# Kernel tuning notes

Hardware: AMD Instinct MI355X
Metric: run time of the kernel (lower is better)

Reference implementation:

```python
import jax, jax.numpy as jnp
import numpy as np

# Model dims (match init_kwargs)
B, S, D = 4, 2048, 1024          # batch, seq, d_model
H, E, DH = 8, 4, 128             # n_heads, n_experts_attn, d_head
K = 2                            # k_attn (routed, n_expert_shared_attn=0)
NEG_INF = jnp.float32(-1e30)


def setup_inputs() -> dict:
    key = jax.random.key(0)
    ks = jax.random.split(key, 9)
    s = np.float32(1.0 / np.sqrt(D))
    return {
        "q_src": jax.random.normal(ks[0], (B, S, D), jnp.float32),
        "k_src": jax.random.normal(ks[1], (B, S, D), jnp.float32),
        "v_src": jax.random.normal(ks[2], (B, S, D), jnp.float32),
        "wq": jax.random.normal(ks[3], (H * DH, D), jnp.float32) * s,
        "wk": jax.random.normal(ks[4], (H * DH, D), jnp.float32) * s,
        "sel_v_w": jax.random.normal(ks[5], (H * E, D), jnp.float32) * s,
        "sel_o_w": jax.random.normal(ks[6], (H * E, D), jnp.float32) * s,
        "v_w": jax.random.normal(ks[7], (H, E, D, DH), jnp.float32) * s,
        "o_w": jax.random.normal(ks[8], (H, E, DH, D), jnp.float32) * np.float32(1.0 / np.sqrt(H * DH)),
        "bias_v": jnp.zeros((E,), jnp.float32),   # load-balancing bias buffer (zeros at init)
        "bias_o": jnp.zeros((E,), jnp.float32),
        # causal boolean mask, True = attend (skip_mask all True -> trimming is identity)
        "attn_mask": jnp.broadcast_to(jnp.tril(jnp.ones((S, S), bool)), (B, S, S)),
        "position_ids": jnp.broadcast_to(jnp.arange(S, dtype=jnp.int32), (B, S)),
        "skip_mask": jnp.ones((B, S), bool),
    }


def _expert_gate(x, w, bias):
    """Sigmoid gating + per-head top-k routed expert selection.
    Returns dense combine weights [b,s,h,E] (sum of sel_val * one_hot) and indices [b,s,h,K]."""
    logits = (x @ w.T).reshape(*x.shape[:-1], H, E)        # [b,s,h,E]
    sel = jax.nn.sigmoid(logits)
    # bias only affects *which* experts are picked (added under no_grad in torch)
    _, idx = jax.lax.top_k(jax.lax.stop_gradient(sel) + bias, K)  # [b,s,h,K]
    sel_val = jnp.take_along_axis(sel, idx, axis=-1)        # [b,s,h,K]
    gate = jnp.sum(jax.nn.one_hot(idx, E, dtype=sel.dtype) * sel_val[..., None], axis=-2)
    return gate, idx


def reference(q_src, k_src, v_src, wq, wk, sel_v_w, sel_o_w, v_w, o_w,
              bias_v, bias_o, attn_mask, position_ids, skip_mask):
    # scale.sqrt() applied to both q and k -> full 1/sqrt(d_head) on scores
    ssq = jnp.float32((1.0 / np.sqrt(DH)) ** 0.5)
    q = ((q_src @ wq.T) * ssq).reshape(B, S, H, DH).transpose(0, 2, 1, 3)  # [b,h,s,dh]
    k = ((k_src @ wk.T) * ssq).reshape(B, S, H, DH).transpose(0, 2, 1, 3)

    v_gate, v_idx = _expert_gate(k_src, sel_v_w, bias_v)    # V experts routed on k_src
    o_gate, o_idx = _expert_gate(q_src, sel_o_w, bias_o)    # O experts routed on q_src

    # expert-mixed V projection (cvmm): all experts then dense combine
    all_v = jnp.einsum('bsm,hemd->bshed', v_src, v_w)       # [b,s,h,E,dh]
    v = jnp.einsum('bshed,bshe->bhsd', all_v, v_gate)       # [b,h,s,dh]

    scores = jnp.einsum('bhqd,bhkd->bhqk', q, k)
    scores = jnp.where(attn_mask[:, None], scores, NEG_INF)
    attn = jax.nn.softmax(scores, axis=-1)
    out = jnp.einsum('bhqk,bhkd->bqhd', attn, v)            # [b,s,h,dh]

    # expert-mixed O projection, summed over heads
    scaled = out[..., None, :] * o_gate[..., None]          # [b,s,h,E,dh]
    res = jnp.einsum('bshed,hedm->bsm', scaled, o_w)        # [b,s,d_model]
    return res, (v_idx, o_idx)
```

## Files before the change

### kernel.cpp

```cpp
#include <hip/hip_runtime.h>
#include <cstdint>
#include <cstddef>

typedef __bf16 bf16;
typedef __bf16 bf16x4 __attribute__((ext_vector_type(4)));
typedef __bf16 bf16x8 __attribute__((ext_vector_type(8)));
typedef float  fx4    __attribute__((ext_vector_type(4)));


__device__ __forceinline__ void async16(const bf16* g, bf16* l) {
  __builtin_amdgcn_global_load_lds((const __attribute__((address_space(1))) void*)g,
                                   (__attribute__((address_space(3))) void*)l, 16, 0, 0);
}

template <int CTRL>
__device__ __forceinline__ float dppf(float x) {
  return __int_as_float(__builtin_amdgcn_update_dpp(
      0, __float_as_int(x), CTRL, 0xf, 0xf, true));
}

__global__ __launch_bounds__(256) void f32_to_bf16(const float4* __restrict__ src,
                                                   bf16x4* __restrict__ dst, int n4) {
  int i = blockIdx.x * 256 + threadIdx.x;
  if (i < n4) {
    float4 v = src[i];
    bf16x4 o;
    o[0] = (bf16)v.x; o[1] = (bf16)v.y; o[2] = (bf16)v.z; o[3] = (bf16)v.w;
    dst[i] = o;
  }
}

__global__ __launch_bounds__(256) void make_wvt(const float* __restrict__ v_w,
                                                bf16* __restrict__ wvt) {
  __shared__ float tile[64][65];
  const int he = blockIdx.z, k0 = blockIdx.x * 64, dh0 = blockIdx.y * 64;
  const float* in = v_w + (size_t)he * 1024 * 128;
  #pragma unroll
  for (int j = 0; j < 16; j++) {
    int idx = threadIdx.x + j * 256;
    int r = idx >> 6, c = idx & 63;
    tile[r][c] = in[(size_t)(k0 + r) * 128 + dh0 + c];
  }
  __syncthreads();
  const int h = he >> 2, e = he & 3;
  bf16* outp = wvt + ((size_t)(h * 128 + dh0) * 4 + e) * 1024 + k0;
  #pragma unroll
  for (int j = 0; j < 16; j++) {
    int idx = threadIdx.x + j * 256;
    int r = idx >> 6, c = idx & 63;
    outp[(size_t)r * 4096 + c] = (bf16)tile[c][r];
  }
}

__global__ __launch_bounds__(256) void make_wot(const float* __restrict__ o_w,
                                                bf16* __restrict__ wot) {
  __shared__ float tile[64][65];
  const int he = blockIdx.z, d0 = blockIdx.x * 64, dh0 = blockIdx.y * 64;
  const float* in = o_w + (size_t)he * 128 * 1024;
  #pragma unroll
  for (int j = 0; j < 16; j++) {
    int idx = threadIdx.x + j * 256;
    int r = idx >> 6, c = idx & 63;
    tile[r][c] = in[(size_t)(dh0 + r) * 1024 + d0 + c];
  }
  __syncthreads();
  bf16* outp = wot + (size_t)d0 * 4096 + he * 128 + dh0;
  #pragma unroll
  for (int j = 0; j < 16; j++) {
    int idx = threadIdx.x + j * 256;
    int r = idx >> 6, c = idx & 63;
    outp[(size_t)r * 4096 + c] = (bf16)tile[c][r];
  }
}

__global__ __launch_bounds__(256) void gating(const float* __restrict__ q_src,
                                              const float* __restrict__ k_src,
                                              const float* __restrict__ sel_v_w,
                                              const float* __restrict__ sel_o_w,
                                              const float* __restrict__ bias_v,
                                              const float* __restrict__ bias_o,
                                              float* __restrict__ gate_v,
                                              float* __restrict__ gate_o,
                                              float* __restrict__ d_out) {
  int m = blockIdx.x, g = blockIdx.y;
  const float* x = g ? q_src : k_src;
  const float* w = g ? sel_o_w : sel_v_w;
  const float* bias = g ? bias_o : bias_v;
  float* gate = g ? gate_o : gate_v;
  float* idxo = d_out + 8388608 + g * 131072;

  __shared__ float xs[1024];
  __shared__ double part_s[32][8];
  __shared__ double sel_s[32];
  int t = threadIdx.x;
  #pragma unroll
  for (int p = 0; p < 4; p++) xs[t + p * 256] = x[(size_t)m * 1024 + t + p * 256];
  __syncthreads();
  int he = t >> 3, pp = t & 7;
  const float* wrow = w + he * 1024;
  double acc = 0.0;
  for (int j = 0; j < 128; j++) { int k = pp + j * 8; acc += (double)xs[k] * (double)wrow[k]; }
  part_s[he][pp] = acc;
  __syncthreads();
  if (t < 32) {
    double tot = 0.0;
    #pragma unroll
    for (int j = 0; j < 8; j++) tot += part_s[t][j];
    sel_s[t] = 1.0 / (1.0 + exp(-tot));
  }
  __syncthreads();
  if (t < 8) {
    double v[4], vbv[4];
    #pragma unroll
    for (int e = 0; e < 4; e++) { v[e] = sel_s[t * 4 + e]; vbv[e] = v[e] + (double)bias[e]; }
    int i0 = 0;
    for (int e = 1; e < 4; e++) if (vbv[e] > vbv[i0]) i0 = e;
    int i1 = -1; double best = -1e300;
    for (int e = 0; e < 4; e++) { if (e == i0) continue; if (vbv[e] > best) { best = vbv[e]; i1 = e; } }
    float* gp = gate + ((size_t)m * 8 + t) * 4;
    #pragma unroll
    for (int e = 0; e < 4; e++) {
      float gv = 0.f;
      if (e == i0) gv = (float)v[i0];
      else if (e == i1) gv = (float)v[i1];
      gp[e] = gv;
    }
    idxo[m * 16 + t * 2 + 0] = (float)i0;
    idxo[m * 16 + t * 2 + 1] = (float)i1;
  }
}

__global__ __launch_bounds__(256) void expand_o(const bf16* __restrict__ outb,
                                                const float* __restrict__ gate_o,
                                                bf16* __restrict__ Ae) {
  int idx = blockIdx.x * 256 + threadIdx.x;
  int m = idx >> 9;
  int u = idx & 511;
  int he = u >> 4;
  int hh = he >> 2, e = he & 3;
  int dh0 = (u & 15) * 8;
  float gv = gate_o[((size_t)m * 8 + hh) * 4 + e];
  bf16x8 v = *(const bf16x8*)(outb + ((size_t)m * 8 + hh) * 128 + dh0);
  #pragma unroll
  for (int j = 0; j < 8; j++) v[j] = (bf16)((float)v[j] * gv);
  *(bf16x8*)(Ae + (size_t)m * 4096 + u * 8) = v;
}

template <int MODE>
__global__ __launch_bounds__(256) void gemm_moe(const bf16* __restrict__ Abf,
                                                const bf16* __restrict__ BT,
                                                const float* __restrict__ gate,
                                                bf16* __restrict__ Cbf,
                                                float* __restrict__ Cf32,
                                                float scale) {
  constexpr int KDIM = (MODE == 0) ? 1024 : 4096;
  constexpr int ASTRIDE = (MODE == 2) ? 4096 : 1024;
  __shared__ __align__(16) bf16 smem[32768];
  const int t = threadIdx.x;
  const int wave = t >> 6, lane = t & 63;
  const int wr = wave >> 1, wc = wave & 1;
  const int quad = lane >> 4, l16 = lane & 15;
  const int m0 = blockIdx.y * 128;
  const int n0 = blockIdx.x * 128;
  const int h = (MODE == 1) ? blockIdx.z : 0;
  const bf16* BTh = (MODE == 1) ? BT + (size_t)h * 128 * 4096 : BT;

  fx4 acc[4][4] = {};
  fx4 accT[4][4] = {};

  const int drow = lane >> 3, dch = lane & 7;

  auto stage = [&](int buf, int k0) {
    bf16* As = smem + buf * 16384;
    bf16* Bs = As + 8192;
    #pragma unroll
    for (int p = 0; p < 4; p++) {
      int row = p * 32 + wave * 8 + drow;
      int sc = dch ^ (row & 7);
      async16(BTh + (size_t)(n0 + row) * KDIM + k0 + sc * 8,
              Bs + row * 64 + dch * 8);
    }
    int col = (MODE == 1) ? (k0 & 1023) : k0;
    #pragma unroll
    for (int p = 0; p < 4; p++) {
      int row = p * 32 + wave * 8 + drow;
      int sc = dch ^ (row & 7);
      async16(Abf + (size_t)(m0 + row) * ASTRIDE + col + sc * 8,
              As + row * 64 + dch * 8);
    }
  };

  stage(0, 0);
  int buf = 0;
  for (int k0 = 0; k0 < KDIM; k0 += 64) {
    if (k0 + 64 < KDIM) {
      stage(buf ^ 1, k0 + 64);
      asm volatile("s_waitcnt vmcnt(8)" ::: "memory");
    } else {
      asm volatile("s_waitcnt vmcnt(0)" ::: "memory");
    }
    __builtin_amdgcn_s_barrier();
    asm volatile("" ::: "memory");
    const bf16* As = smem + buf * 16384;
    const bf16* Bs = As + 8192;
    #pragma unroll
    for (int kk = 0; kk < 64; kk += 32) {
      bf16x8 af[4], bfr[4];
      #pragma unroll
      for (int i = 0; i < 4; i++) {
        int ar = wr * 64 + i * 16 + l16;
        af[i]  = *(const bf16x8*)(As + ar * 64 + ((((kk >> 3) + quad) ^ (ar & 7)) * 8));
      }
      #pragma unroll
      for (int i = 0; i < 4; i++) {
        int br = wc * 64 + i * 16 + l16;
        bfr[i] = *(const bf16x8*)(Bs + br * 64 + ((((kk >> 3) + quad) ^ (br & 7)) * 8));
      }
      #pragma unroll
      for (int mi = 0; mi < 4; mi++)
        #pragma unroll
        for (int ni = 0; ni < 4; ni++)
          acc[mi][ni] = __builtin_amdgcn_mfma_f32_16x16x32_bf16(af[mi], bfr[ni], acc[mi][ni], 0, 0, 0);
    }
    if constexpr (MODE == 1) {
      if (((k0 + 64) & 1023) == 0) {
        const int e = k0 >> 10;
        #pragma unroll
        for (int mi = 0; mi < 4; mi++)
          #pragma unroll
          for (int r = 0; r < 4; r++) {
            int m = m0 + wr * 64 + mi * 16 + quad * 4 + r;
            float gv = gate[((size_t)m * 8 + h) * 4 + e];
            #pragma unroll
            for (int ni = 0; ni < 4; ni++)
              accT[mi][ni][r] += gv * acc[mi][ni][r];
          }
        #pragma unroll
        for (int mi = 0; mi < 4; mi++)
          #pragma unroll
          for (int ni = 0; ni < 4; ni++)
            #pragma unroll
            for (int j = 0; j < 4; j++) acc[mi][ni][j] = 0.f;
      }
    }
    asm volatile("" ::: "memory");
    __builtin_amdgcn_s_barrier();
    buf ^= 1;
  }

  if (MODE == 1) {
    #pragma unroll
    for (int mi = 0; mi < 4; mi++)
      #pragma unroll
      for (int ni = 0; ni < 4; ni++) {
        int nl = wc * 64 + ni * 16 + l16;
        int ml = wr * 64 + mi * 16 + quad * 4;
        bf16x4 pk;
        #pragma unroll
        for (int r = 0; r < 4; r++) pk[r] = (bf16)accT[mi][ni][r];
        *(bf16x4*)(smem + nl * 136 + ml) = pk;
      }
    __syncthreads();
    int b = m0 >> 11, s0 = m0 & 2047;
    const int row = t >> 1, base = (t & 1) * 64;
    bf16* dst = Cbf + (((size_t)(b * 8 + h) * 128) + row) * 2048 + s0 + base;
    #pragma unroll
    for (int j = 0; j < 8; j++)
      *(float4*)(dst + j * 8) = *(float4*)(smem + row * 136 + base + j * 8);
    return;
  }

  #pragma unroll
  for (int mi = 0; mi < 4; mi++)
    #pragma unroll
    for (int ni = 0; ni < 4; ni++)
      #pragma unroll
      for (int r = 0; r < 4; r++) {
        int m = m0 + wr * 64 + mi * 16 + quad * 4 + r;
        int n = n0 + wc * 64 + ni * 16 + l16;
        float v = acc[mi][ni][r] * scale;
        if (MODE == 0) {
          int b = m >> 11, s = m & 2047, hh = n >> 7, dh = n & 127;
          Cbf[(((size_t)(b * 8 + hh) * 2048 + s) << 7) + dh] = (bf16)v;
        } else {
          Cf32[(size_t)m * 1024 + n] = v;
        }
      }
}

__global__ __launch_bounds__(256) void attn_kernel(const bf16* __restrict__ qb,
                                                   const bf16* __restrict__ kb,
                                                   const bf16* __restrict__ vbT,
                                                   bf16* __restrict__ outb) {
  const int bh = blockIdx.y;
  const int b = bh >> 3, h = bh & 7;
  __shared__ __align__(16) bf16 Ks[2][64 * 128];
  __shared__ __align__(16) bf16 VTs[2][128 * 64];
  __shared__ __align__(16) bf16 Ps[4][16][72];
  const int t = threadIdx.x, wave = t >> 6, lane = t & 63;
  const int quad = lane >> 4, l16 = lane & 15;
  const bf16* qbase  = qb  + (size_t)bh * 2048 * 128;
  const bf16* kbase  = kb  + (size_t)bh * 2048 * 128;
  const bf16* vtbase = vbT + (size_t)bh * 128 * 2048;

  auto stage = [&](int buf, int kt) {
    #pragma unroll
    for (int p = 0; p < 4; p++) {
      int o = p * 4096 + wave * 1024 + lane * 16;
      int kr = o >> 8, kc = o & 255;
      async16((const bf16*)((const char*)kbase + (size_t)(kt * 64 + kr) * 256 + (kc ^ ((kr & 7) << 4))),
              (bf16*)((char*)&Ks[buf][0] + o));
    }
    #pragma unroll
    for (int p = 0; p < 4; p++) {
      int o = p * 4096 + wave * 1024 + lane * 16;
      int vr = o >> 7, vc = o & 127;
      async16((const bf16*)((const char*)vtbase + (size_t)vr * 4096 + kt * 128 + (vc ^ ((vr & 7) << 4))),
              (bf16*)((char*)&VTs[buf][0] + o));
    }
  };

  #pragma unroll 1
  for (int pass = 0; pass < 2; pass++) {
    const int qt = pass ? blockIdx.x : (31 - blockIdx.x);

    bf16x8 qf[4];
    #pragma unroll
    for (int dk = 0; dk < 4; dk++)
      qf[dk] = *(const bf16x8*)(qbase + (size_t)(qt * 64 + wave * 16 + l16) * 128 + dk * 32 + quad * 8);

    float m_run[4], l_run[4];
    fx4 acc_o[8] = {};
    #pragma unroll
    for (int r = 0; r < 4; r++) { m_run[r] = -1e30f; l_run[r] = 0.f; }

    stage(0, 0);
    int cur = 0;

    for (int kt = 0; kt <= qt; kt++) {
      if (kt < qt) {
        stage(cur ^ 1, kt + 1);
        asm volatile("s_waitcnt vmcnt(8)" ::: "memory");
      } else {
        asm volatile("s_waitcnt vmcnt(0)" ::: "memory");
      }
      __builtin_amdgcn_s_barrier();
      asm volatile("" ::: "memory");

      const char* Ksb  = (const char*)&Ks[cur][0];
      const char* VTsb = (const char*)&VTs[cur][0];

      fx4 accs[4] = {};
      __builtin_amdgcn_s_setprio(1);
      #pragma unroll
      for (int ni = 0; ni < 4; ni++)
        #pragma unroll
        for (int dk = 0; dk < 4; dk++) {
          int r = ni * 16 + l16;
          bf16x8 kf = *(const bf16x8*)(Ksb + r * 256 + ((dk * 64 + quad * 16) ^ ((r & 7) << 4)));
          accs[ni] = __builtin_amdgcn_mfma_f32_16x16x32_bf16(qf[dk], kf, accs[ni], 0, 0, 0);
        }
      __builtin_amdgcn_s_setprio(0);

      if (kt == qt) {
        #pragma unroll
        for (int ni = 0; ni < 4; ni++)
          #pragma unroll
          for (int r = 0; r < 4; r++) {
            int qr = wave * 16 + quad * 4 + r;
            int kc = ni * 16 + l16;
            if (kc > qr) accs[ni][r] = -1e30f;
          }
      }

      #pragma unroll
      for (int r = 0; r < 4; r++) {
        float mx = fmaxf(fmaxf(accs[0][r], accs[1][r]), fmaxf(accs[2][r], accs[3][r]));
        mx = fmaxf(mx, dppf<0x121>(mx));
        mx = fmaxf(mx, dppf<0x122>(mx));
        mx = fmaxf(mx, dppf<0x124>(mx));
        mx = fmaxf(mx, dppf<0x128>(mx));
        float m_new = fmaxf(m_run[r], mx);
        float alpha = __builtin_amdgcn_exp2f(m_run[r] - m_new);
        float rs = 0.f;
        #pragma unroll
        for (int ni = 0; ni < 4; ni++) {
          float p = __builtin_amdgcn_exp2f(accs[ni][r] - m_new);
          accs[ni][r] = p; rs += p;
        }
        rs += dppf<0x121>(rs);
        rs += dppf<0x122>(rs);
        rs += dppf<0x124>(rs);
        rs += dppf<0x128>(rs);
        l_run[r] = l_run[r] * alpha + rs;
        m_run[r] = m_new;
        #pragma unroll
        for (int nj = 0; nj < 8; nj++) acc_o[nj][r] *= alpha;
      }

      #pragma unroll
      for (int ni = 0; ni < 4; ni++)
        #pragma unroll
        for (int r = 0; r < 4; r++)
          Ps[wave][quad * 4 + r][ni * 16 + l16] = (bf16)accs[ni][r];

      __builtin_amdgcn_s_setprio(1);
      #pragma unroll
      for (int step = 0; step < 2; step++) {
        bf16x8 pf = *(const bf16x8*)&Ps[wave][l16][step * 32 + quad * 8];
        #pragma unroll
        for (int nj = 0; nj < 8; nj++) {
          int r = nj * 16 + l16;
          bf16x8 vf = *(const bf16x8*)(VTsb + r * 128 + ((step * 64 + quad * 16) ^ ((r & 7) << 4)));
          acc_o[nj] = __builtin_amdgcn_mfma_f32_16x16x32_bf16(pf, vf, acc_o[nj], 0, 0, 0);
        }
      }
      __builtin_amdgcn_s_setprio(0);

      asm volatile("" ::: "memory");
      __builtin_amdgcn_s_barrier();
      cur ^= 1;
    }

    #pragma unroll
    for (int nj = 0; nj < 8; nj++)
      #pragma unroll
      for (int r = 0; r < 4; r++) {
        int s = qt * 64 + wave * 16 + quad * 4 + r;
        int token = b * 2048 + s;
        float o = acc_o[nj][r] / l_run[r];
        outb[((size_t)token * 8 + h) * 128 + nj * 16 + l16] = (bf16)o;
      }
  }
}

extern "C" void kernel_launch(void* const* d_in, const int* in_sizes, int n_in,
                              void* d_out, int out_size, void* d_ws, size_t ws_size,
                              hipStream_t stream) {
  const float* q_src  = (const float*)d_in[0];
  const float* k_src  = (const float*)d_in[1];
  const float* v_src  = (const float*)d_in[2];
  const float* wq     = (const float*)d_in[3];
  const float* wk     = (const float*)d_in[4];
  const float* sel_v_w = (const float*)d_in[5];
  const float* sel_o_w = (const float*)d_in[6];
  const float* v_w    = (const float*)d_in[7];
  const float* o_w    = (const float*)d_in[8];
  const float* bias_v = (const float*)d_in[9];
  const float* bias_o = (const float*)d_in[10];
  float* out = (float*)d_out;

  char* ws = (char*)d_ws;
  size_t off = 0;
  auto alloc = [&](size_t bytes) { char* p = ws + off; off += (bytes + 255) & ~(size_t)255; return p; };
  bf16* wqb   = (bf16*)alloc((size_t)1024 * 1024 * 2);
  bf16* wkb   = (bf16*)alloc((size_t)1024 * 1024 * 2);
  bf16* wvt   = (bf16*)alloc((size_t)8 * 128 * 4 * 1024 * 2);
  bf16* wot   = (bf16*)alloc((size_t)1024 * 4096 * 2);
  float* gate_v = (float*)alloc((size_t)8192 * 32 * 4);
  float* gate_o = (float*)alloc((size_t)8192 * 32 * 4);
  bf16* qsb   = (bf16*)alloc((size_t)8192 * 1024 * 2);
  bf16* ksb   = (bf16*)alloc((size_t)8192 * 1024 * 2);
  bf16* vsb   = (bf16*)alloc((size_t)8192 * 1024 * 2);
  bf16* qb    = (bf16*)alloc((size_t)8192 * 1024 * 2);
  bf16* kb    = (bf16*)alloc((size_t)8192 * 1024 * 2);
  bf16* vbT   = (bf16*)alloc((size_t)8192 * 1024 * 2);
  bf16* outb  = (bf16*)alloc((size_t)8192 * 1024 * 2);
  bf16* Ae    = qsb;

  f32_to_bf16<<<1024, 256, 0, stream>>>((const float4*)wq, (bf16x4*)wqb, 262144);
  f32_to_bf16<<<1024, 256, 0, stream>>>((const float4*)wk, (bf16x4*)wkb, 262144);
  f32_to_bf16<<<8192, 256, 0, stream>>>((const float4*)q_src, (bf16x4*)qsb, 2097152);
  f32_to_bf16<<<8192, 256, 0, stream>>>((const float4*)k_src, (bf16x4*)ksb, 2097152);
  f32_to_bf16<<<8192, 256, 0, stream>>>((const float4*)v_src, (bf16x4*)vsb, 2097152);
  make_wvt<<<dim3(16, 2, 32), 256, 0, stream>>>(v_w, wvt);
  make_wot<<<dim3(16, 2, 32), 256, 0, stream>>>(o_w, wot);
  gating<<<dim3(8192, 2), 256, 0, stream>>>(q_src, k_src, sel_v_w, sel_o_w,
                                            bias_v, bias_o, gate_v, gate_o, out);

  const float ssq = 0.29730177875068026f;
  const float log2e = 1.4426950408889634f;
  gemm_moe<0><<<dim3(8, 64), 256, 0, stream>>>(qsb, wqb, nullptr, qb, nullptr, ssq * log2e);
  gemm_moe<0><<<dim3(8, 64), 256, 0, stream>>>(ksb, wkb, nullptr, kb, nullptr, ssq);
  gemm_moe<1><<<dim3(1, 64, 8), 256, 0, stream>>>(vsb, wvt, gate_v, vbT, nullptr, 1.0f);
  attn_kernel<<<dim3(16, 32), 256, 0, stream>>>(qb, kb, vbT, outb);
  expand_o<<<16384, 256, 0, stream>>>(outb, gate_o, Ae);
  gemm_moe<2><<<dim3(8, 64), 256, 0, stream>>>(Ae, wot, nullptr, nullptr, out, 1.0f);
}
```

Baseline: 692.8 us.

## Enlarge MoE GEMM tiles to 256x128 with 8 waves and ping-pong MFMA scheduling

The projection GEMMs now use 512-thread blocks, each covering a 256x128 output tile, with the B tile in its own shared-memory region. The launch becomes a 1D grid of 256 blocks. The inner loop splits MFMA work into two halves separated by barriers and raises wave priority during MFMA, so that LDS reads from some waves overlap math in others. The aim is better reuse of the B operand and better MFMA utilization, at the cost of more LDS, extra barriers, and fewer blocks than the 256 CUs can hold.

```diff
diff --git a/kernel.cpp b/kernel.cpp
--- a/kernel.cpp
+++ b/kernel.cpp
@@ -12,6 +12,9 @@
   __builtin_amdgcn_global_load_lds((const __attribute__((address_space(1))) void*)g,
                                    (__attribute__((address_space(3))) void*)l, 16, 0, 0);
 }
+
+#define BARRIER() do { asm volatile("" ::: "memory"); __builtin_amdgcn_s_barrier(); \
+                       asm volatile("" ::: "memory"); } while (0)
 
 template <int CTRL>
 __device__ __forceinline__ float dppf(float x) {
@@ -147,7 +150,7 @@
 }
 
 template <int MODE>
-__global__ __launch_bounds__(256) void gemm_moe(const bf16* __restrict__ Abf,
+__global__ __launch_bounds__(512) void gemm_moe(const bf16* __restrict__ Abf,
                                                 const bf16* __restrict__ BT,
                                                 const float* __restrict__ gate,
                                                 bf16* __restrict__ Cbf,
@@ -155,38 +158,39 @@
                                                 float scale) {
   constexpr int KDIM = (MODE == 0) ? 1024 : 4096;
   constexpr int ASTRIDE = (MODE == 2) ? 4096 : 1024;
-  __shared__ __align__(16) bf16 smem[32768];
+  __shared__ __align__(16) bf16 smem[49152];
   const int t = threadIdx.x;
   const int wave = t >> 6, lane = t & 63;
   const int wr = wave >> 1, wc = wave & 1;
   const int quad = lane >> 4, l16 = lane & 15;
-  const int m0 = blockIdx.y * 128;
-  const int n0 = blockIdx.x * 128;
-  const int h = (MODE == 1) ? blockIdx.z : 0;
+  const int bid = blockIdx.x;
+  const int m0 = (bid >> 3) * 256;
+  const int n0 = (MODE == 1) ? 0 : (bid & 7) * 128;
+  const int h = (MODE == 1) ? (bid & 7) : 0;
   const bf16* BTh = (MODE == 1) ? BT + (size_t)h * 128 * 4096 : BT;
 
   fx4 acc[4][4] = {};
   fx4 accT[4][4] = {};
 
-  const int drow = lane >> 3, dch = lane & 7;
+  const int srow = t >> 3, sch = t & 7;
 
   auto stage = [&](int buf, int k0) {
     bf16* As = smem + buf * 16384;
-    bf16* Bs = As + 8192;
+    bf16* Bs = smem + 32768 + buf * 8192;
+    #pragma unroll
+    for (int p = 0; p < 2; p++) {
+      int row = p * 64 + srow;
+      int sc = sch ^ (row & 7);
+      async16(BTh + (size_t)(n0 + row) * KDIM + k0 + sc * 8,
+              Bs + row * 64 + sch * 8);
+    }
+    int col = (MODE == 1) ? (k0 & 1023) : k0;
     #pragma unroll
     for (int p = 0; p < 4; p++) {
-      int row = p * 32 + wave * 8 + drow;
-      int sc = dch ^ (row & 7);
-      async16(BTh + (size_t)(n0 + row) * KDIM + k0 + sc * 8,
-              Bs + row * 64 + dch * 8);
-    }
-    int col = (MODE == 1) ? (k0 & 1023) : k0;
-    #pragma unroll
-    for (int p = 0; p < 4; p++) {
-      int row = p * 32 + wave * 8 + drow;
-      int sc = dch ^ (row & 7);
+      int row = p * 64 + srow;
+      int sc = sch ^ (row & 7);
       async16(Abf + (size_t)(m0 + row) * ASTRIDE + col + sc * 8,
-              As + row * 64 + dch * 8);
+              As + row * 64 + sch * 8);
     }
   };
 
@@ -195,32 +199,49 @@
   for (int k0 = 0; k0 < KDIM; k0 += 64) {
     if (k0 + 64 < KDIM) {
       stage(buf ^ 1, k0 + 64);
-      asm volatile("s_waitcnt vmcnt(8)" ::: "memory");
+      asm volatile("s_waitcnt vmcnt(6)" ::: "memory");
     } else {
       asm volatile("s_waitcnt vmcnt(0)" ::: "memory");
     }
-    __builtin_amdgcn_s_barrier();
-    asm volatile("" ::: "memory");
+    BARRIER();
     const bf16* As = smem + buf * 16384;
-    const bf16* Bs = As + 8192;
+    const bf16* Bs = smem + 32768 + buf * 8192;
     #pragma unroll
     for (int kk = 0; kk < 64; kk += 32) {
       bf16x8 af[4], bfr[4];
       #pragma unroll
       for (int i = 0; i < 4; i++) {
         int ar = wr * 64 + i * 16 + l16;
-        af[i]  = *(const bf16x8*)(As + ar * 64 + ((((kk >> 3) + quad) ^ (ar & 7)) * 8));
-      }
-      #pragma unroll
-      for (int i = 0; i < 4; i++) {
+        af[i] = *(const bf16x8*)(As + ar * 64 + ((((kk >> 3) + quad) ^ (ar & 7)) * 8));
+      }
+      #pragma unroll
+      for (int i = 0; i < 2; i++) {
         int br = wc * 64 + i * 16 + l16;
         bfr[i] = *(const bf16x8*)(Bs + br * 64 + ((((kk >> 3) + quad) ^ (br & 7)) * 8));
       }
+      BARRIER();
+      __builtin_amdgcn_s_setprio(1);
       #pragma unroll
       for (int mi = 0; mi < 4; mi++)
         #pragma unroll
-        for (int ni = 0; ni < 4; ni++)
+        for (int ni = 0; ni < 2; ni++)
           acc[mi][ni] = __builtin_amdgcn_mfma_f32_16x16x32_bf16(af[mi], bfr[ni], acc[mi][ni], 0, 0, 0);
+      __builtin_amdgcn_s_setprio(0);
+      BARRIER();
+      #pragma unroll
+      for (int i = 2; i < 4; i++) {
+        int br = wc * 64 + i * 16 + l16;
+        bfr[i] = *(const bf16x8*)(Bs + br * 64 + ((((kk >> 3) + quad) ^ (br & 7)) * 8));
+      }
+      BARRIER();
+      __builtin_amdgcn_s_setprio(1);
+      #pragma unroll
+      for (int mi = 0; mi < 4; mi++)
+        #pragma unroll
+        for (int ni = 2; ni < 4; ni++)
+          acc[mi][ni] = __builtin_amdgcn_mfma_f32_16x16x32_bf16(af[mi], bfr[ni], acc[mi][ni], 0, 0, 0);
+      __builtin_amdgcn_s_setprio(0);
+      BARRIER();
     }
     if constexpr (MODE == 1) {
       if (((k0 + 64) & 1023) == 0) {
@@ -243,8 +264,6 @@
             for (int j = 0; j < 4; j++) acc[mi][ni][j] = 0.f;
       }
     }
-    asm volatile("" ::: "memory");
-    __builtin_amdgcn_s_barrier();
     buf ^= 1;
   }
 
@@ -258,15 +277,15 @@
         bf16x4 pk;
         #pragma unroll
         for (int r = 0; r < 4; r++) pk[r] = (bf16)accT[mi][ni][r];
-        *(bf16x4*)(smem + nl * 136 + ml) = pk;
+        *(bf16x4*)(smem + nl * 264 + ml) = pk;
       }
     __syncthreads();
     int b = m0 >> 11, s0 = m0 & 2047;
-    const int row = t >> 1, base = (t & 1) * 64;
-    bf16* dst = Cbf + (((size_t)(b * 8 + h) * 128) + row) * 2048 + s0 + base;
+    const int row = t >> 2, seg = t & 3;
+    bf16* dst = Cbf + (((size_t)(b * 8 + h) * 128) + row) * 2048 + s0 + seg * 64;
     #pragma unroll
     for (int j = 0; j < 8; j++)
-      *(float4*)(dst + j * 8) = *(float4*)(smem + row * 136 + base + j * 8);
+      *(float4*)(dst + j * 8) = *(float4*)(smem + row * 264 + seg * 64 + j * 8);
     return;
   }
 
@@ -480,10 +499,10 @@
 
   const float ssq = 0.29730177875068026f;
   const float log2e = 1.4426950408889634f;
-  gemm_moe<0><<<dim3(8, 64), 256, 0, stream>>>(qsb, wqb, nullptr, qb, nullptr, ssq * log2e);
-  gemm_moe<0><<<dim3(8, 64), 256, 0, stream>>>(ksb, wkb, nullptr, kb, nullptr, ssq);
-  gemm_moe<1><<<dim3(1, 64, 8), 256, 0, stream>>>(vsb, wvt, gate_v, vbT, nullptr, 1.0f);
+  gemm_moe<0><<<256, 512, 0, stream>>>(qsb, wqb, nullptr, qb, nullptr, ssq * log2e);
+  gemm_moe<0><<<256, 512, 0, stream>>>(ksb, wkb, nullptr, kb, nullptr, ssq);
+  gemm_moe<1><<<256, 512, 0, stream>>>(vsb, wvt, gate_v, vbT, nullptr, 1.0f);
   attn_kernel<<<dim3(16, 32), 256, 0, stream>>>(qb, kb, vbT, outb);
   expand_o<<<16384, 256, 0, stream>>>(outb, gate_o, Ae);
-  gemm_moe<2><<<dim3(8, 64), 256, 0, stream>>>(Ae, wot, nullptr, nullptr, out, 1.0f);
-}
+  gemm_moe<2><<<256, 512, 0, stream>>>(Ae, wot, nullptr, nullptr, out, 1.0f);
+}
```

Result: faster. 646.8 us (-6.6%).
